# Kernel tuning notes

Measured on AMD Instinct MI355X. Metric: run time of the kernel, lower is better.

## Reference

```python
import jax, jax.numpy as jnp
import numpy as np
from jax import lax

B, N, C_IN, H, W = 256, 64, 3, 8, 8
CH = [32, 64, 128]   # cnn channels per stage
D = 128              # fc / gnn width
OUT = 5
BN_EPS = 1e-5


def setup_inputs() -> dict:
    key = jax.random.key(0)
    ks = jax.random.split(key, 24)
    x = jax.random.normal(ks[0], (B, N, C_IN, H, W), jnp.float32)
    # sparse symmetric communication graph, no self loops (GCNConv adds them)
    a = jax.random.uniform(ks[1], (B, N, N)) < 0.15
    a = jnp.logical_or(a, jnp.swapaxes(a, 1, 2)).astype(jnp.float32)
    gso = a * (1.0 - jnp.eye(N, dtype=jnp.float32))

    def lin(k, o, i):
        return (jax.random.normal(k, (o, i), jnp.float32) / np.sqrt(i)).astype(jnp.float32)

    def conv(k, o, i):
        return (jax.random.normal(k, (o, i, 3, 3), jnp.float32) / np.sqrt(i * 9)).astype(jnp.float32)

    inp = {
        'x': x, 'gso': gso,
        'w_c1': conv(ks[2], CH[0], C_IN), 'b_c1': jnp.zeros((CH[0],), jnp.float32),
        'g_bn1': jnp.ones((CH[0],), jnp.float32), 'be_bn1': jnp.zeros((CH[0],), jnp.float32),
        'w_c2': conv(ks[3], CH[1], CH[0]), 'b_c2': jnp.zeros((CH[1],), jnp.float32),
        'g_bn2': jnp.ones((CH[1],), jnp.float32), 'be_bn2': jnp.zeros((CH[1],), jnp.float32),
        'w_c3': conv(ks[4], CH[2], CH[1]), 'b_c3': jnp.zeros((CH[2],), jnp.float32),
        'g_bn3': jnp.ones((CH[2],), jnp.float32), 'be_bn3': jnp.zeros((CH[2],), jnp.float32),
        'w_fc': lin(ks[5], D, CH[2]), 'b_fc': jnp.zeros((D,), jnp.float32),
        'w_g1': lin(ks[6], D, D), 'b_g1': jnp.zeros((D,), jnp.float32),
        'w_g2': lin(ks[7], D, D), 'b_g2': jnp.zeros((D,), jnp.float32),
        'w_out': lin(ks[8], OUT, D), 'b_out': jnp.zeros((OUT,), jnp.float32),
    }
    return inp


def _cnn_block(h, w, b, g, be):
    h = lax.conv_general_dilated(h, w, (1, 1), 'SAME',
                                 dimension_numbers=('NCHW', 'OIHW', 'NCHW'))
    h = h + b[None, :, None, None]
    # eval-mode BatchNorm2d with running_mean=0, running_var=1
    h = h * (g / jnp.sqrt(1.0 + BN_EPS))[None, :, None, None] + be[None, :, None, None]
    h = jax.nn.relu(h)
    h = lax.reduce_window(h, -jnp.inf, lax.max, (1, 1, 2, 2), (1, 1, 2, 2), 'VALID')
    return h


def _forward(x, gso, w_c1, b_c1, g_bn1, be_bn1, w_c2, b_c2, g_bn2, be_bn2,
             w_c3, b_c3, g_bn3, be_bn3, w_fc, b_fc, w_g1, b_g1, w_g2, b_g2,
             w_out, b_out):
    b, n = x.shape[0], x.shape[1]
    h = x.reshape(b * n, x.shape[2], x.shape[3], x.shape[4])  # vectorize agents
    h = _cnn_block(h, w_c1, b_c1, g_bn1, be_bn1)
    h = _cnn_block(h, w_c2, b_c2, g_bn2, be_bn2)
    h = _cnn_block(h, w_c3, b_c3, g_bn3, be_bn3)          # [B*N, CH2, 1, 1]
    h = h.reshape(b * n, -1)
    h = jax.nn.relu(h @ w_fc.T + b_fc)                    # [B*N, D]
    feat = h.reshape(b, n, -1)
    # GCNConv: add self loops (weight 1), symmetric normalization
    a1 = gso + jnp.eye(n, dtype=gso.dtype)
    dinv = lax.rsqrt(a1.sum(-1))                          # deg >= 1
    ahat = dinv[:, :, None] * a1 * dinv[:, None, :]       # [B, N, N]
    hg = jax.nn.relu(jnp.einsum('bij,bjf->bif', ahat, feat @ w_g1.T) + b_g1)
    hg = jax.nn.relu(jnp.einsum('bij,bjf->bif', ahat, hg @ w_g2.T) + b_g2)
    actions = hg @ w_out.T + b_out                        # [B, N, OUT]
    return actions


def reference(x, gso, w_c1, b_c1, g_bn1, be_bn1, w_c2, b_c2, g_bn2, be_bn2,
              w_c3, b_c3, g_bn3, be_bn3, w_fc, b_fc, w_g1, b_g1, w_g2, b_g2,
              w_out, b_out):
    return _forward(x, gso, w_c1, b_c1, g_bn1, be_bn1, w_c2, b_c2, g_bn2, be_bn2,
                    w_c3, b_c3, g_bn3, be_bn3, w_fc, b_fc, w_g1, b_g1, w_g2, b_g2,
                    w_out, b_out)
```

## Files before the change

kernel.cpp:

```cpp
#include <hip/hip_runtime.h>
#include <math.h>


typedef __attribute__((ext_vector_type(8))) short bf16x8;
typedef __attribute__((ext_vector_type(4))) float f32x4;

__device__ __forceinline__ short f2bf(float f) {
  union { float f; unsigned u; } v; v.f = f;
  unsigned r = v.u + 0x7fffu + ((v.u >> 16) & 1u);
  return (short)(r >> 16);
}
__device__ __forceinline__ float bf2f(unsigned short u) {
  union { unsigned u; float f; } v; v.u = ((unsigned)u) << 16;
  return v.f;
}

__global__ __launch_bounds__(256) void pack_all(
    const float* __restrict__ w_c1, const float* __restrict__ w_c2,
    const float* __restrict__ w_c3, const float* __restrict__ w_fc,
    const float* __restrict__ w_g1, const float* __restrict__ w_g2,
    short* __restrict__ B1, short* __restrict__ B2, short* __restrict__ B3,
    short* __restrict__ Wfc, short* __restrict__ Wg1, short* __restrict__ Wg2) {
  int idx = blockIdx.x * 256 + threadIdx.x;
  if (idx < 2048) {
    int oc = idx >> 6, k = idx & 63;
    int t = k >> 2, ic = k & 3;
    float v = (t < 9 && ic < 3) ? w_c1[(oc * 3 + ic) * 9 + t] : 0.0f;
    B1[idx] = f2bf(v);
  } else if (idx < 20480) {
    int i2 = idx - 2048;
    int oc = i2 / 288, r = i2 - oc * 288;
    int t = r >> 5, ic = r & 31;
    B2[i2] = f2bf(w_c2[(oc * 32 + ic) * 9 + t]);
  } else if (idx < 94208) {
    int i3 = idx - 20480;
    int oc = i3 / 576, r = i3 - oc * 576;
    int t = r >> 6, ic = r & 63;
    B3[i3] = f2bf(w_c3[(oc * 64 + ic) * 9 + t]);
  } else if (idx < 110592) {
    int i = idx - 94208; Wfc[i] = f2bf(w_fc[i]);
  } else if (idx < 126976) {
    int i = idx - 110592; Wg1[i] = f2bf(w_g1[i]);
  } else if (idx < 143360) {
    int i = idx - 126976; Wg2[i] = f2bf(w_g2[i]);
  }
}

__global__ __launch_bounds__(256) void conv1_mfma(
    const float* __restrict__ x, const short* __restrict__ B1,
    const float* __restrict__ bias, const float* __restrict__ g,
    const float* __restrict__ be, short* __restrict__ c1) {
  __shared__ short sx[8 * 400];
  const int tid = threadIdx.x;
  const int s0 = blockIdx.x * 8;
  for (int i = tid; i < 400; i += 256)
    *(uint4*)(sx + i * 8) = (uint4){0, 0, 0, 0};
  __syncthreads();
  for (int p = tid; p < 512; p += 256) {
    const int si = p >> 6, pix = p & 63;
    const int y = pix >> 3, xx2 = pix & 7;
    const float* xb = x + (s0 + si) * 192 + pix;
    ushort4 o;
    o.x = (unsigned short)f2bf(xb[0]);
    o.y = (unsigned short)f2bf(xb[64]);
    o.z = (unsigned short)f2bf(xb[128]);
    o.w = 0;
    *(ushort4*)(sx + si * 400 + ((y + 1) * 10 + xx2 + 1) * 4) = o;
  }
  __syncthreads();
  const int lane = tid & 63, w = tid >> 6;
  const int col = lane & 15, quad = lane >> 4;
  bf16x8 Bf[2][2];
#pragma unroll
  for (int nt = 0; nt < 2; ++nt)
#pragma unroll
    for (int ks = 0; ks < 2; ++ks)
      Bf[nt][ks] = *(const bf16x8*)(B1 + (nt * 16 + col) * 64 + ks * 32 + quad * 8);
  float Abn[2], Cbn[2];
#pragma unroll
  for (int nt = 0; nt < 2; ++nt) {
    int oc = nt * 16 + col;
    float a = g[oc] * rsqrtf(1.0f + 1e-5f);
    Abn[nt] = a;
    Cbn[nt] = fmaf(bias[oc], a, be[oc]);
  }
  const int t0 = 2 * quad, t1 = t0 + 1;
  const int ky0 = t0 / 3, kx0 = t0 - 3 * (t0 / 3);
  const int ky1 = t1 / 3, kx1 = t1 - 3 * (t1 / 3);
  const int m = lane & 15;
  const int pl = m >> 2, sub = m & 3;
  const int dy = sub >> 1, dx = sub & 1;
  const uint2 z2 = {0u, 0u};
#pragma unroll
  for (int sl = 0; sl < 2; ++sl) {
    const int si = w * 2 + sl;
    const int s = s0 + si;
    const short* xb = sx + si * 400;
#pragma unroll
    for (int tile = 0; tile < 4; ++tile) {
      const int pi = tile * 4 + pl;
      const int py = pi >> 2, px = pi & 3;
      const int cy = 2 * py + dy, cx = 2 * px + dx;
      union { bf16x8 v; uint2 u[2]; } a0, a1;
      a0.u[0] = *(const uint2*)(xb + ((cy + ky0) * 10 + cx + kx0) * 4);
      a0.u[1] = *(const uint2*)(xb + ((cy + ky1) * 10 + cx + kx1) * 4);
      uint2 u8 = *(const uint2*)(xb + ((cy + 2) * 10 + cx + 2) * 4);
      a1.u[0] = (quad == 0) ? u8 : z2;
      a1.u[1] = z2;
      f32x4 acc0 = {0, 0, 0, 0}, acc1 = {0, 0, 0, 0};
      acc0 = __builtin_amdgcn_mfma_f32_16x16x32_bf16(a0.v, Bf[0][0], acc0, 0, 0, 0);
      acc0 = __builtin_amdgcn_mfma_f32_16x16x32_bf16(a1.v, Bf[0][1], acc0, 0, 0, 0);
      acc1 = __builtin_amdgcn_mfma_f32_16x16x32_bf16(a0.v, Bf[1][0], acc1, 0, 0, 0);
      acc1 = __builtin_amdgcn_mfma_f32_16x16x32_bf16(a1.v, Bf[1][1], acc1, 0, 0, 0);
      const int piq = tile * 4 + quad;
#pragma unroll
      for (int nt = 0; nt < 2; ++nt) {
        f32x4 acc = nt ? acc1 : acc0;
        float p0 = fmaf(acc[0], Abn[nt], Cbn[nt]);
        float p1 = fmaf(acc[1], Abn[nt], Cbn[nt]);
        float p2 = fmaf(acc[2], Abn[nt], Cbn[nt]);
        float p3 = fmaf(acc[3], Abn[nt], Cbn[nt]);
        float mx = fmaxf(fmaxf(fmaxf(p0, p1), fmaxf(p2, p3)), 0.0f);
        c1[s * 512 + piq * 32 + nt * 16 + col] = f2bf(mx);
      }
    }
  }
}

__global__ __launch_bounds__(256, 2) void conv2_mfma(
    const short* __restrict__ c1, const short* __restrict__ B2,
    const float* __restrict__ bias, const float* __restrict__ g,
    const float* __restrict__ be, short* __restrict__ c2) {
  __shared__ short sx[32 * 640];
  const int tid = threadIdx.x;
  const int s0 = blockIdx.x * 32;
#pragma unroll
  for (int it = 0; it < 8; ++it) {
    int c = it * 256 + tid;
    int s_l = c >> 6, k = c & 63;
    int cell = k >> 2, seg = k & 3;
    *(bf16x8*)(sx + s_l * 640 + cell * 40 + seg * 8) =
        *(const bf16x8*)(c1 + s0 * 512 + c * 8);
  }
  const int lane = tid & 63, w = tid >> 6;
  const int col = lane & 15, quad = lane >> 4;
  bf16x8 Bf[4][9];
#pragma unroll
  for (int nt = 0; nt < 4; ++nt)
#pragma unroll
    for (int t = 0; t < 9; ++t)
      Bf[nt][t] = *(const bf16x8*)(B2 + (nt * 16 + col) * 288 + t * 32 + quad * 8);
  float Abn[4], Cbn[4];
#pragma unroll
  for (int nt = 0; nt < 4; ++nt) {
    int oc = nt * 16 + col;
    float a = g[oc] * rsqrtf(1.0f + 1e-5f);
    Abn[nt] = a;
    Cbn[nt] = fmaf(bias[oc], a, be[oc]);
  }
  const int m = lane & 15;
  const int q2 = m >> 2, sub = m & 3;
  const int cy = 2 * (q2 >> 1) + (sub >> 1);
  const int cx = 2 * (q2 & 1) + (sub & 1);
  int off[9];
  bool valid[9];
#pragma unroll
  for (int t = 0; t < 9; ++t) {
    int ky = t / 3, kx = t - 3 * (t / 3);
    int yy = cy + ky - 1, xx = cx + kx - 1;
    valid[t] = ((unsigned)yy < 4u) && ((unsigned)xx < 4u);
    int yc = min(max(yy, 0), 3), xc = min(max(xx, 0), 3);
    off[t] = (yc * 4 + xc) * 40 + quad * 8;
  }
  const bf16x8 zf = {0, 0, 0, 0, 0, 0, 0, 0};
  __syncthreads();
#pragma unroll 1
  for (int si = 0; si < 8; ++si) {
    const int s_l = w * 8 + si;
    const short* ib = sx + s_l * 640;
    f32x4 acc[4];
#pragma unroll
    for (int nt = 0; nt < 4; ++nt) acc[nt] = (f32x4){0, 0, 0, 0};
#pragma unroll
    for (int t = 0; t < 9; ++t) {
      bf16x8 a = *(const bf16x8*)(ib + off[t]);
      if (!valid[t]) a = zf;
#pragma unroll
      for (int nt = 0; nt < 4; ++nt)
        acc[nt] = __builtin_amdgcn_mfma_f32_16x16x32_bf16(a, Bf[nt][t], acc[nt], 0, 0, 0);
    }
    short* ob = c2 + (s0 + s_l) * 256;
#pragma unroll
    for (int nt = 0; nt < 4; ++nt) {
      float p0 = fmaf(acc[nt][0], Abn[nt], Cbn[nt]);
      float p1 = fmaf(acc[nt][1], Abn[nt], Cbn[nt]);
      float p2 = fmaf(acc[nt][2], Abn[nt], Cbn[nt]);
      float p3 = fmaf(acc[nt][3], Abn[nt], Cbn[nt]);
      float mx = fmaxf(fmaxf(fmaxf(p0, p1), fmaxf(p2, p3)), 0.0f);
      ob[quad * 64 + nt * 16 + col] = f2bf(mx);
    }
  }
}

__global__ __launch_bounds__(256) void conv3_mfma(
    const short* __restrict__ c2, const short* __restrict__ B3,
    const float* __restrict__ bias, const float* __restrict__ g,
    const float* __restrict__ be, short* __restrict__ c3) {
  __shared__ short sB[32 * 584];
  __shared__ short sA[16 * 296];
  const int tid = threadIdx.x;
  const int s0 = blockIdx.x * 16;
#pragma unroll
  for (int it = 0; it < 2; ++it) {
    int c = it * 256 + tid;
    int s_l = c >> 5, k = c & 31;
    int cell = k >> 3, seg = k & 7;
    *(bf16x8*)(sA + s_l * 296 + cell * 72 + seg * 8) =
        *(const bf16x8*)(c2 + s0 * 256 + c * 8);
  }
  __syncthreads();
  const int lane = tid & 63, w = tid >> 6;
  const int col = lane & 15, quad = lane >> 4;
  const int m = lane & 15;
  const int cp = m & 3, sl = m >> 2;
  const int cy = cp >> 1, cx = cp & 1;
  const short* ib = sA + (w * 4 + sl) * 296;
  bf16x8 A[18];
  const bf16x8 zf = {0, 0, 0, 0, 0, 0, 0, 0};
#pragma unroll
  for (int ks = 0; ks < 18; ++ks) {
    int t = ks >> 1;
    int ky = t / 3, kx = t - 3 * (t / 3);
    int iy = cy + ky - 1, ix = cx + kx - 1;
    bool valid = ((unsigned)iy < 2u) && ((unsigned)ix < 2u);
    int iyc = min(max(iy, 0), 1), ixc = min(max(ix, 0), 1);
    bf16x8 a = *(const bf16x8*)(ib + (iyc * 2 + ixc) * 72 + (ks & 1) * 32 + quad * 8);
    A[ks] = valid ? a : zf;
  }
  f32x4 acc[8];
#pragma unroll
  for (int i = 0; i < 8; ++i) acc[i] = (f32x4){0, 0, 0, 0};
#pragma unroll
  for (int ng = 0; ng < 4; ++ng) {
    __syncthreads();
#pragma unroll
    for (int it = 0; it < 9; ++it) {
      int cidx = it * 256 + tid;
      int row = cidx / 72, seg = cidx - row * 72;
      *(bf16x8*)(sB + row * 584 + seg * 8) =
          *(const bf16x8*)(B3 + (ng * 32 + row) * 576 + seg * 8);
    }
    __syncthreads();
#pragma unroll
    for (int nt = 0; nt < 2; ++nt) {
      const int nB = (nt * 16 + col) * 584 + quad * 8;
#pragma unroll
      for (int ks = 0; ks < 18; ++ks) {
        bf16x8 b = *(const bf16x8*)(sB + nB + ks * 32);
        acc[ng * 2 + nt] =
            __builtin_amdgcn_mfma_f32_16x16x32_bf16(A[ks], b, acc[ng * 2 + nt], 0, 0, 0);
      }
    }
  }
  const int sample = s0 + w * 4 + quad;
#pragma unroll
  for (int i = 0; i < 8; ++i) {
    int oc = (i >> 1) * 32 + (i & 1) * 16 + col;
    float a = g[oc] * rsqrtf(1.0f + 1e-5f);
    float cc = fmaf(bias[oc], a, be[oc]);
    float p0 = fmaf(acc[i][0], a, cc);
    float p1 = fmaf(acc[i][1], a, cc);
    float p2 = fmaf(acc[i][2], a, cc);
    float p3 = fmaf(acc[i][3], a, cc);
    float mx = fmaxf(fmaxf(fmaxf(p0, p1), fmaxf(p2, p3)), 0.0f);
    c3[sample * 128 + oc] = f2bf(mx);
  }
}

__global__ __launch_bounds__(512) void fused_dense(
    const short* __restrict__ c3, const float* __restrict__ gso,
    const short* __restrict__ Wfc, const short* __restrict__ Wg1,
    const short* __restrict__ Wg2, const float* __restrict__ b_fc,
    const float* __restrict__ b_g1, const float* __restrict__ b_g2,
    const float* __restrict__ w_o, const float* __restrict__ b_o,
    float* __restrict__ out) {
  __shared__ short sAct[64 * 136];
  __shared__ short sT[128 * 72];
  __shared__ short sAhat[64 * 72];
  __shared__ float sDinv[64];
  __shared__ float sWo[640];
  const int tid = threadIdx.x;
  const int b = blockIdx.x;
  float* sG = (float*)sT;
  for (int i = tid; i < 4096; i += 512) sG[i] = gso[b * 4096 + i];
  for (int i = tid; i < 640; i += 512) sWo[i] = w_o[i];
  __syncthreads();
  if (tid < 64) {
    float ssum = 1.0f;
    for (int j = 0; j < 64; ++j) ssum += sG[j * 64 + tid];
    sDinv[tid] = rsqrtf(ssum);
  }
  __syncthreads();
  for (int i = tid; i < 4096; i += 512) {
    int r = i >> 6, c = i & 63;
    float v = sDinv[r] * (sG[i] + (r == c ? 1.0f : 0.0f)) * sDinv[c];
    sAhat[r * 72 + c] = f2bf(v);
  }
  for (int i = tid; i < 1024; i += 512) {
    int r = i >> 4, seg = i & 15;
    *(bf16x8*)(sAct + r * 136 + seg * 8) =
        *(const bf16x8*)(c3 + (b * 64 + r) * 128 + seg * 8);
  }
  __syncthreads();
  const int lane = tid & 63, w8 = tid >> 6;
  const int rg = w8 >> 1, nh = w8 & 1;
  const int col = lane & 15, quad = lane >> 4;
  const int arow = (rg * 16 + col) * 136;
  const int crow0 = (rg * 16 + quad * 4) * 136;
  bf16x8 A[4];
  f32x4 acc[4];

#pragma unroll
  for (int ks = 0; ks < 4; ++ks)
    A[ks] = *(const bf16x8*)(sAct + arow + ks * 32 + quad * 8);
  __syncthreads();
#pragma unroll
  for (int i = 0; i < 4; ++i) acc[i] = (f32x4){0, 0, 0, 0};
#pragma unroll
  for (int ntl = 0; ntl < 4; ++ntl) {
    const int n = (nh * 4 + ntl) * 16 + col;
#pragma unroll
    for (int ks = 0; ks < 4; ++ks) {
      bf16x8 bb = *(const bf16x8*)(Wfc + n * 128 + ks * 32 + quad * 8);
      acc[ntl] = __builtin_amdgcn_mfma_f32_16x16x32_bf16(A[ks], bb, acc[ntl], 0, 0, 0);
    }
  }
#pragma unroll
  for (int ntl = 0; ntl < 4; ++ntl) {
    const int n = (nh * 4 + ntl) * 16 + col;
    const float bv = b_fc[n];
#pragma unroll
    for (int reg = 0; reg < 4; ++reg)
      sAct[crow0 + reg * 136 + n] = f2bf(fmaxf(acc[ntl][reg] + bv, 0.0f));
  }
  __syncthreads();

#pragma unroll
  for (int ks = 0; ks < 4; ++ks)
    A[ks] = *(const bf16x8*)(sAct + arow + ks * 32 + quad * 8);
#pragma unroll
  for (int i = 0; i < 4; ++i) acc[i] = (f32x4){0, 0, 0, 0};
#pragma unroll
  for (int ntl = 0; ntl < 4; ++ntl) {
    const int n = (nh * 4 + ntl) * 16 + col;
#pragma unroll
    for (int ks = 0; ks < 4; ++ks) {
      bf16x8 bb = *(const bf16x8*)(Wg1 + n * 128 + ks * 32 + quad * 8);
      acc[ntl] = __builtin_amdgcn_mfma_f32_16x16x32_bf16(A[ks], bb, acc[ntl], 0, 0, 0);
    }
  }
#pragma unroll
  for (int ntl = 0; ntl < 4; ++ntl) {
    const int n = (nh * 4 + ntl) * 16 + col;
    ushort4 pk;
    pk.x = (unsigned short)f2bf(acc[ntl][0]);
    pk.y = (unsigned short)f2bf(acc[ntl][1]);
    pk.z = (unsigned short)f2bf(acc[ntl][2]);
    pk.w = (unsigned short)f2bf(acc[ntl][3]);
    *(ushort4*)(sT + n * 72 + rg * 16 + quad * 4) = pk;
  }
  __syncthreads();

  bf16x8 Ah[2];
#pragma unroll
  for (int ks = 0; ks < 2; ++ks)
    Ah[ks] = *(const bf16x8*)(sAhat + (rg * 16 + col) * 72 + ks * 32 + quad * 8);
#pragma unroll
  for (int i = 0; i < 4; ++i) acc[i] = (f32x4){0, 0, 0, 0};
#pragma unroll
  for (int ntl = 0; ntl < 4; ++ntl) {
    const int n = (nh * 4 + ntl) * 16 + col;
#pragma unroll
    for (int ks = 0; ks < 2; ++ks) {
      bf16x8 bb = *(const bf16x8*)(sT + n * 72 + ks * 32 + quad * 8);
      acc[ntl] = __builtin_amdgcn_mfma_f32_16x16x32_bf16(Ah[ks], bb, acc[ntl], 0, 0, 0);
    }
  }
#pragma unroll
  for (int ntl = 0; ntl < 4; ++ntl) {
    const int n = (nh * 4 + ntl) * 16 + col;
    const float bv = b_g1[n];
#pragma unroll
    for (int reg = 0; reg < 4; ++reg)
      sAct[crow0 + reg * 136 + n] = f2bf(fmaxf(acc[ntl][reg] + bv, 0.0f));
  }
  __syncthreads();

#pragma unroll
  for (int ks = 0; ks < 4; ++ks)
    A[ks] = *(const bf16x8*)(sAct + arow + ks * 32 + quad * 8);
#pragma unroll
  for (int i = 0; i < 4; ++i) acc[i] = (f32x4){0, 0, 0, 0};
#pragma unroll
  for (int ntl = 0; ntl < 4; ++ntl) {
    const int n = (nh * 4 + ntl) * 16 + col;
#pragma unroll
    for (int ks = 0; ks < 4; ++ks) {
      bf16x8 bb = *(const bf16x8*)(Wg2 + n * 128 + ks * 32 + quad * 8);
      acc[ntl] = __builtin_amdgcn_mfma_f32_16x16x32_bf16(A[ks], bb, acc[ntl], 0, 0, 0);
    }
  }
#pragma unroll
  for (int ntl = 0; ntl < 4; ++ntl) {
    const int n = (nh * 4 + ntl) * 16 + col;
    ushort4 pk;
    pk.x = (unsigned short)f2bf(acc[ntl][0]);
    pk.y = (unsigned short)f2bf(acc[ntl][1]);
    pk.z = (unsigned short)f2bf(acc[ntl][2]);
    pk.w = (unsigned short)f2bf(acc[ntl][3]);
    *(ushort4*)(sT + n * 72 + rg * 16 + quad * 4) = pk;
  }
  __syncthreads();

#pragma unroll
  for (int i = 0; i < 4; ++i) acc[i] = (f32x4){0, 0, 0, 0};
#pragma unroll
  for (int ntl = 0; ntl < 4; ++ntl) {
    const int n = (nh * 4 + ntl) * 16 + col;
#pragma unroll
    for (int ks = 0; ks < 2; ++ks) {
      bf16x8 bb = *(const bf16x8*)(sT + n * 72 + ks * 32 + quad * 8);
      acc[ntl] = __builtin_amdgcn_mfma_f32_16x16x32_bf16(Ah[ks], bb, acc[ntl], 0, 0, 0);
    }
  }
#pragma unroll
  for (int ntl = 0; ntl < 4; ++ntl) {
    const int n = (nh * 4 + ntl) * 16 + col;
    const float bv = b_g2[n];
#pragma unroll
    for (int reg = 0; reg < 4; ++reg)
      sAct[crow0 + reg * 136 + n] = f2bf(fmaxf(acc[ntl][reg] + bv, 0.0f));
  }
  __syncthreads();

  if (tid < 320) {
    const int j = tid / 5, o = tid - 5 * j;
    float a0 = 0.0f;
#pragma unroll
    for (int k8 = 0; k8 < 16; ++k8) {
      union { bf16x8 v; unsigned short u[8]; } h;
      h.v = *(const bf16x8*)(sAct + j * 136 + k8 * 8);
#pragma unroll
      for (int jj = 0; jj < 8; ++jj)
        a0 = fmaf(bf2f(h.u[jj]), sWo[o * 128 + k8 * 8 + jj], a0);
    }
    out[(b * 64 + j) * 5 + o] = a0 + b_o[o];
  }
}

extern "C" void kernel_launch(void* const* d_in, const int* in_sizes, int n_in,
                              void* d_out, int out_size, void* d_ws, size_t ws_size,
                              hipStream_t stream) {
  const float* x    = (const float*)d_in[0];
  const float* gso  = (const float*)d_in[1];
  const float* w_c1 = (const float*)d_in[2];
  const float* b_c1 = (const float*)d_in[3];
  const float* g_b1 = (const float*)d_in[4];
  const float* e_b1 = (const float*)d_in[5];
  const float* w_c2 = (const float*)d_in[6];
  const float* b_c2 = (const float*)d_in[7];
  const float* g_b2 = (const float*)d_in[8];
  const float* e_b2 = (const float*)d_in[9];
  const float* w_c3 = (const float*)d_in[10];
  const float* b_c3 = (const float*)d_in[11];
  const float* g_b3 = (const float*)d_in[12];
  const float* e_b3 = (const float*)d_in[13];
  const float* w_fc = (const float*)d_in[14];
  const float* b_fc = (const float*)d_in[15];
  const float* w_g1 = (const float*)d_in[16];
  const float* b_g1 = (const float*)d_in[17];
  const float* w_g2 = (const float*)d_in[18];
  const float* b_g2 = (const float*)d_in[19];
  const float* w_o  = (const float*)d_in[20];
  const float* b_o  = (const float*)d_in[21];
  float* out = (float*)d_out;
  char* ws = (char*)d_ws;

  short* c1  = (short*)(ws + 0);
  short* c2  = (short*)(ws + 16777216);
  short* c3  = (short*)(ws + 25165824);
  short* B1  = (short*)(ws + 29360128);
  short* B2  = (short*)(ws + 29364224);
  short* B3  = (short*)(ws + 29401088);
  short* Wfc = (short*)(ws + 29548544);
  short* Wg1 = (short*)(ws + 29581312);
  short* Wg2 = (short*)(ws + 29614080);

  pack_all<<<560, 256, 0, stream>>>(w_c1, w_c2, w_c3, w_fc, w_g1, w_g2,
                                    B1, B2, B3, Wfc, Wg1, Wg2);
  conv1_mfma<<<2048, 256, 0, stream>>>(x, B1, b_c1, g_b1, e_b1, c1);
  conv2_mfma<<<512, 256, 0, stream>>>(c1, B2, b_c2, g_b2, e_b2, c2);
  conv3_mfma<<<1024, 256, 0, stream>>>(c2, B3, b_c3, g_b3, e_b3, c3);
  fused_dense<<<256, 512, 0, stream>>>(c3, gso, Wfc, Wg1, Wg2, b_fc, b_g1,
                                       b_g2, w_o, b_o, out);
}
```

Baseline: 181.1 us.

## Fuse three conv stages into one kernel keeping intermediates in LDS

Merges conv1, conv2 and conv3 into a single kernel processing 16 samples per block, with the pooled intermediate activations held in shared memory instead of global workspace. This removes the global write and read of the c1 and c2 tensors and two kernel launches. In exchange, each block reloads the conv2 weights and stages the conv3 weights in smaller chunks with more barriers. Register and LDS pressure rise and may lower occupancy.

Result: faster. 177.1 us (-2.2%).

```diff
diff --git a/kernel.cpp b/kernel.cpp
--- a/kernel.cpp
+++ b/kernel.cpp
@@ -46,234 +46,203 @@
   }
 }
 
-__global__ __launch_bounds__(256) void conv1_mfma(
-    const float* __restrict__ x, const short* __restrict__ B1,
-    const float* __restrict__ bias, const float* __restrict__ g,
-    const float* __restrict__ be, short* __restrict__ c1) {
-  __shared__ short sx[8 * 400];
+__global__ __launch_bounds__(256, 2) void conv_all(
+    const float* __restrict__ x, const short* __restrict__ B1g,
+    const short* __restrict__ B2g, const short* __restrict__ B3g,
+    const float* __restrict__ b1, const float* __restrict__ g1,
+    const float* __restrict__ e1, const float* __restrict__ b2,
+    const float* __restrict__ g2, const float* __restrict__ e2,
+    const float* __restrict__ b3, const float* __restrict__ g3,
+    const float* __restrict__ e3, short* __restrict__ c3) {
+  __shared__ short sMix[16 * 584];
+  __shared__ short sc1[16 * 640];
+  __shared__ short sc2[16 * 296];
   const int tid = threadIdx.x;
-  const int s0 = blockIdx.x * 8;
-  for (int i = tid; i < 400; i += 256)
-    *(uint4*)(sx + i * 8) = (uint4){0, 0, 0, 0};
-  __syncthreads();
-  for (int p = tid; p < 512; p += 256) {
-    const int si = p >> 6, pix = p & 63;
-    const int y = pix >> 3, xx2 = pix & 7;
+  const int s0 = blockIdx.x * 16;
+  const int lane = tid & 63, w = tid >> 6;
+  const int col = lane & 15, quad = lane >> 4;
+  const int m = lane & 15;
+
+  for (int i = tid; i < 800; i += 256)
+    *(uint4*)(sMix + i * 8) = (uint4){0, 0, 0, 0};
+  __syncthreads();
+#pragma unroll
+  for (int it = 0; it < 4; ++it) {
+    int p = it * 256 + tid;
+    int si = p >> 6, pix = p & 63;
+    int y = pix >> 3, xx2 = pix & 7;
     const float* xb = x + (s0 + si) * 192 + pix;
     ushort4 o;
     o.x = (unsigned short)f2bf(xb[0]);
     o.y = (unsigned short)f2bf(xb[64]);
     o.z = (unsigned short)f2bf(xb[128]);
     o.w = 0;
-    *(ushort4*)(sx + si * 400 + ((y + 1) * 10 + xx2 + 1) * 4) = o;
-  }
-  __syncthreads();
-  const int lane = tid & 63, w = tid >> 6;
-  const int col = lane & 15, quad = lane >> 4;
-  bf16x8 Bf[2][2];
-#pragma unroll
-  for (int nt = 0; nt < 2; ++nt)
-#pragma unroll
-    for (int ks = 0; ks < 2; ++ks)
-      Bf[nt][ks] = *(const bf16x8*)(B1 + (nt * 16 + col) * 64 + ks * 32 + quad * 8);
-  float Abn[2], Cbn[2];
-#pragma unroll
-  for (int nt = 0; nt < 2; ++nt) {
-    int oc = nt * 16 + col;
-    float a = g[oc] * rsqrtf(1.0f + 1e-5f);
-    Abn[nt] = a;
-    Cbn[nt] = fmaf(bias[oc], a, be[oc]);
-  }
-  const int t0 = 2 * quad, t1 = t0 + 1;
-  const int ky0 = t0 / 3, kx0 = t0 - 3 * (t0 / 3);
-  const int ky1 = t1 / 3, kx1 = t1 - 3 * (t1 / 3);
-  const int m = lane & 15;
-  const int pl = m >> 2, sub = m & 3;
-  const int dy = sub >> 1, dx = sub & 1;
-  const uint2 z2 = {0u, 0u};
-#pragma unroll
-  for (int sl = 0; sl < 2; ++sl) {
-    const int si = w * 2 + sl;
-    const int s = s0 + si;
-    const short* xb = sx + si * 400;
-#pragma unroll
-    for (int tile = 0; tile < 4; ++tile) {
-      const int pi = tile * 4 + pl;
-      const int py = pi >> 2, px = pi & 3;
-      const int cy = 2 * py + dy, cx = 2 * px + dx;
-      union { bf16x8 v; uint2 u[2]; } a0, a1;
-      a0.u[0] = *(const uint2*)(xb + ((cy + ky0) * 10 + cx + kx0) * 4);
-      a0.u[1] = *(const uint2*)(xb + ((cy + ky1) * 10 + cx + kx1) * 4);
-      uint2 u8 = *(const uint2*)(xb + ((cy + 2) * 10 + cx + 2) * 4);
-      a1.u[0] = (quad == 0) ? u8 : z2;
-      a1.u[1] = z2;
-      f32x4 acc0 = {0, 0, 0, 0}, acc1 = {0, 0, 0, 0};
-      acc0 = __builtin_amdgcn_mfma_f32_16x16x32_bf16(a0.v, Bf[0][0], acc0, 0, 0, 0);
-      acc0 = __builtin_amdgcn_mfma_f32_16x16x32_bf16(a1.v, Bf[0][1], acc0, 0, 0, 0);
-      acc1 = __builtin_amdgcn_mfma_f32_16x16x32_bf16(a0.v, Bf[1][0], acc1, 0, 0, 0);
-      acc1 = __builtin_amdgcn_mfma_f32_16x16x32_bf16(a1.v, Bf[1][1], acc1, 0, 0, 0);
-      const int piq = tile * 4 + quad;
-#pragma unroll
-      for (int nt = 0; nt < 2; ++nt) {
-        f32x4 acc = nt ? acc1 : acc0;
-        float p0 = fmaf(acc[0], Abn[nt], Cbn[nt]);
-        float p1 = fmaf(acc[1], Abn[nt], Cbn[nt]);
-        float p2 = fmaf(acc[2], Abn[nt], Cbn[nt]);
-        float p3 = fmaf(acc[3], Abn[nt], Cbn[nt]);
+    *(ushort4*)(sMix + si * 400 + ((y + 1) * 10 + xx2 + 1) * 4) = o;
+  }
+  __syncthreads();
+
+  {
+    bf16x8 Bf[2][2];
+#pragma unroll
+    for (int nt = 0; nt < 2; ++nt)
+#pragma unroll
+      for (int ks = 0; ks < 2; ++ks)
+        Bf[nt][ks] = *(const bf16x8*)(B1g + (nt * 16 + col) * 64 + ks * 32 + quad * 8);
+    float Abn[2], Cbn[2];
+#pragma unroll
+    for (int nt = 0; nt < 2; ++nt) {
+      int oc = nt * 16 + col;
+      float a = g1[oc] * rsqrtf(1.0f + 1e-5f);
+      Abn[nt] = a;
+      Cbn[nt] = fmaf(b1[oc], a, e1[oc]);
+    }
+    const int t0 = 2 * quad, t1 = t0 + 1;
+    const int ky0 = t0 / 3, kx0 = t0 - 3 * (t0 / 3);
+    const int ky1 = t1 / 3, kx1 = t1 - 3 * (t1 / 3);
+    const int pl = m >> 2, sub = m & 3;
+    const int dy = sub >> 1, dx = sub & 1;
+    const uint2 z2 = {0u, 0u};
+#pragma unroll
+    for (int sl = 0; sl < 4; ++sl) {
+      const int si = w * 4 + sl;
+      const short* xb = sMix + si * 400;
+#pragma unroll
+      for (int tile = 0; tile < 4; ++tile) {
+        const int pi = tile * 4 + pl;
+        const int py = pi >> 2, px = pi & 3;
+        const int cy = 2 * py + dy, cx = 2 * px + dx;
+        union { bf16x8 v; uint2 u[2]; } a0, a1;
+        a0.u[0] = *(const uint2*)(xb + ((cy + ky0) * 10 + cx + kx0) * 4);
+        a0.u[1] = *(const uint2*)(xb + ((cy + ky1) * 10 + cx + kx1) * 4);
+        uint2 u8 = *(const uint2*)(xb + ((cy + 2) * 10 + cx + 2) * 4);
+        a1.u[0] = (quad == 0) ? u8 : z2;
+        a1.u[1] = z2;
+        f32x4 acc0 = {0, 0, 0, 0}, acc1 = {0, 0, 0, 0};
+        acc0 = __builtin_amdgcn_mfma_f32_16x16x32_bf16(a0.v, Bf[0][0], acc0, 0, 0, 0);
+        acc0 = __builtin_amdgcn_mfma_f32_16x16x32_bf16(a1.v, Bf[0][1], acc0, 0, 0, 0);
+        acc1 = __builtin_amdgcn_mfma_f32_16x16x32_bf16(a0.v, Bf[1][0], acc1, 0, 0, 0);
+        acc1 = __builtin_amdgcn_mfma_f32_16x16x32_bf16(a1.v, Bf[1][1], acc1, 0, 0, 0);
+        const int piq = tile * 4 + quad;
+#pragma unroll
+        for (int nt = 0; nt < 2; ++nt) {
+          f32x4 acc = nt ? acc1 : acc0;
+          float p0 = fmaf(acc[0], Abn[nt], Cbn[nt]);
+          float p1 = fmaf(acc[1], Abn[nt], Cbn[nt]);
+          float p2 = fmaf(acc[2], Abn[nt], Cbn[nt]);
+          float p3 = fmaf(acc[3], Abn[nt], Cbn[nt]);
+          float mx = fmaxf(fmaxf(fmaxf(p0, p1), fmaxf(p2, p3)), 0.0f);
+          sc1[si * 640 + piq * 40 + nt * 16 + col] = f2bf(mx);
+        }
+      }
+    }
+  }
+  __syncthreads();
+
+  {
+    bf16x8 Bf[4][9];
+#pragma unroll
+    for (int nt = 0; nt < 4; ++nt)
+#pragma unroll
+      for (int t = 0; t < 9; ++t)
+        Bf[nt][t] = *(const bf16x8*)(B2g + (nt * 16 + col) * 288 + t * 32 + quad * 8);
+    float Abn[4], Cbn[4];
+#pragma unroll
+    for (int nt = 0; nt < 4; ++nt) {
+      int oc = nt * 16 + col;
+      float a = g2[oc] * rsqrtf(1.0f + 1e-5f);
+      Abn[nt] = a;
+      Cbn[nt] = fmaf(b2[oc], a, e2[oc]);
+    }
+    const int q2 = m >> 2, sub = m & 3;
+    const int cy = 2 * (q2 >> 1) + (sub >> 1);
+    const int cx = 2 * (q2 & 1) + (sub & 1);
+    int off[9];
+    bool valid[9];
+#pragma unroll
+    for (int t = 0; t < 9; ++t) {
+      int ky = t / 3, kx = t - 3 * (t / 3);
+      int yy = cy + ky - 1, xx = cx + kx - 1;
+      valid[t] = ((unsigned)yy < 4u) && ((unsigned)xx < 4u);
+      int yc = min(max(yy, 0), 3), xc = min(max(xx, 0), 3);
+      off[t] = (yc * 4 + xc) * 40 + quad * 8;
+    }
+    const bf16x8 zf = {0, 0, 0, 0, 0, 0, 0, 0};
+#pragma unroll
+    for (int sl = 0; sl < 4; ++sl) {
+      const int si = w * 4 + sl;
+      const short* ib = sc1 + si * 640;
+      f32x4 acc[4];
+#pragma unroll
+      for (int nt = 0; nt < 4; ++nt) acc[nt] = (f32x4){0, 0, 0, 0};
+#pragma unroll
+      for (int t = 0; t < 9; ++t) {
+        bf16x8 a = *(const bf16x8*)(ib + off[t]);
+        if (!valid[t]) a = zf;
+#pragma unroll
+        for (int nt = 0; nt < 4; ++nt)
+          acc[nt] = __builtin_amdgcn_mfma_f32_16x16x32_bf16(a, Bf[nt][t], acc[nt], 0, 0, 0);
+      }
+#pragma unroll
+      for (int nt = 0; nt < 4; ++nt) {
+        float p0 = fmaf(acc[nt][0], Abn[nt], Cbn[nt]);
+        float p1 = fmaf(acc[nt][1], Abn[nt], Cbn[nt]);
+        float p2 = fmaf(acc[nt][2], Abn[nt], Cbn[nt]);
+        float p3 = fmaf(acc[nt][3], Abn[nt], Cbn[nt]);
         float mx = fmaxf(fmaxf(fmaxf(p0, p1), fmaxf(p2, p3)), 0.0f);
-        c1[s * 512 + piq * 32 + nt * 16 + col] = f2bf(mx);
+        sc2[si * 296 + quad * 72 + nt * 16 + col] = f2bf(mx);
       }
     }
   }
-}
-
-__global__ __launch_bounds__(256, 2) void conv2_mfma(
-    const short* __restrict__ c1, const short* __restrict__ B2,
-    const float* __restrict__ bias, const float* __restrict__ g,
-    const float* __restrict__ be, short* __restrict__ c2) {
-  __shared__ short sx[32 * 640];
-  const int tid = threadIdx.x;
-  const int s0 = blockIdx.x * 32;
-#pragma unroll
-  for (int it = 0; it < 8; ++it) {
-    int c = it * 256 + tid;
-    int s_l = c >> 6, k = c & 63;
-    int cell = k >> 2, seg = k & 3;
-    *(bf16x8*)(sx + s_l * 640 + cell * 40 + seg * 8) =
-        *(const bf16x8*)(c1 + s0 * 512 + c * 8);
-  }
-  const int lane = tid & 63, w = tid >> 6;
-  const int col = lane & 15, quad = lane >> 4;
-  bf16x8 Bf[4][9];
-#pragma unroll
-  for (int nt = 0; nt < 4; ++nt)
-#pragma unroll
-    for (int t = 0; t < 9; ++t)
-      Bf[nt][t] = *(const bf16x8*)(B2 + (nt * 16 + col) * 288 + t * 32 + quad * 8);
-  float Abn[4], Cbn[4];
-#pragma unroll
-  for (int nt = 0; nt < 4; ++nt) {
-    int oc = nt * 16 + col;
-    float a = g[oc] * rsqrtf(1.0f + 1e-5f);
-    Abn[nt] = a;
-    Cbn[nt] = fmaf(bias[oc], a, be[oc]);
-  }
-  const int m = lane & 15;
-  const int q2 = m >> 2, sub = m & 3;
-  const int cy = 2 * (q2 >> 1) + (sub >> 1);
-  const int cx = 2 * (q2 & 1) + (sub & 1);
-  int off[9];
-  bool valid[9];
-#pragma unroll
-  for (int t = 0; t < 9; ++t) {
-    int ky = t / 3, kx = t - 3 * (t / 3);
-    int yy = cy + ky - 1, xx = cx + kx - 1;
-    valid[t] = ((unsigned)yy < 4u) && ((unsigned)xx < 4u);
-    int yc = min(max(yy, 0), 3), xc = min(max(xx, 0), 3);
-    off[t] = (yc * 4 + xc) * 40 + quad * 8;
-  }
-  const bf16x8 zf = {0, 0, 0, 0, 0, 0, 0, 0};
-  __syncthreads();
+  __syncthreads();
+
+  {
+    const int cp = m & 3, sl3 = m >> 2;
+    const int cy = cp >> 1, cx = cp & 1;
+    const short* ib = sc2 + (w * 4 + sl3) * 296;
+    bf16x8 A[18];
+    const bf16x8 zf = {0, 0, 0, 0, 0, 0, 0, 0};
+#pragma unroll
+    for (int ks = 0; ks < 18; ++ks) {
+      int t = ks >> 1;
+      int ky = t / 3, kx = t - 3 * (t / 3);
+      int iy = cy + ky - 1, ix = cx + kx - 1;
+      bool valid = ((unsigned)iy < 2u) && ((unsigned)ix < 2u);
+      int iyc = min(max(iy, 0), 1), ixc = min(max(ix, 0), 1);
+      bf16x8 a = *(const bf16x8*)(ib + (iyc * 2 + ixc) * 72 + (ks & 1) * 32 + quad * 8);
+      A[ks] = valid ? a : zf;
+    }
+    f32x4 acc[8];
+#pragma unroll
+    for (int i = 0; i < 8; ++i) acc[i] = (f32x4){0, 0, 0, 0};
 #pragma unroll 1
-  for (int si = 0; si < 8; ++si) {
-    const int s_l = w * 8 + si;
-    const short* ib = sx + s_l * 640;
-    f32x4 acc[4];
-#pragma unroll
-    for (int nt = 0; nt < 4; ++nt) acc[nt] = (f32x4){0, 0, 0, 0};
-#pragma unroll
-    for (int t = 0; t < 9; ++t) {
-      bf16x8 a = *(const bf16x8*)(ib + off[t]);
-      if (!valid[t]) a = zf;
-#pragma unroll
-      for (int nt = 0; nt < 4; ++nt)
-        acc[nt] = __builtin_amdgcn_mfma_f32_16x16x32_bf16(a, Bf[nt][t], acc[nt], 0, 0, 0);
-    }
-    short* ob = c2 + (s0 + s_l) * 256;
-#pragma unroll
-    for (int nt = 0; nt < 4; ++nt) {
-      float p0 = fmaf(acc[nt][0], Abn[nt], Cbn[nt]);
-      float p1 = fmaf(acc[nt][1], Abn[nt], Cbn[nt]);
-      float p2 = fmaf(acc[nt][2], Abn[nt], Cbn[nt]);
-      float p3 = fmaf(acc[nt][3], Abn[nt], Cbn[nt]);
+    for (int ng = 0; ng < 8; ++ng) {
+      __syncthreads();
+      for (int c = tid; c < 1152; c += 256) {
+        int row = c / 72, seg = c - row * 72;
+        *(bf16x8*)(sMix + row * 584 + seg * 8) =
+            *(const bf16x8*)(B3g + (ng * 16 + row) * 576 + seg * 8);
+      }
+      __syncthreads();
+      const int nB = col * 584 + quad * 8;
+#pragma unroll
+      for (int ks = 0; ks < 18; ++ks) {
+        bf16x8 b = *(const bf16x8*)(sMix + nB + ks * 32);
+        acc[ng] = __builtin_amdgcn_mfma_f32_16x16x32_bf16(A[ks], b, acc[ng], 0, 0, 0);
+      }
+    }
+    const int sample = s0 + w * 4 + quad;
+#pragma unroll
+    for (int ng = 0; ng < 8; ++ng) {
+      int oc = ng * 16 + col;
+      float a = g3[oc] * rsqrtf(1.0f + 1e-5f);
+      float cc = fmaf(b3[oc], a, e3[oc]);
+      float p0 = fmaf(acc[ng][0], a, cc);
+      float p1 = fmaf(acc[ng][1], a, cc);
+      float p2 = fmaf(acc[ng][2], a, cc);
+      float p3 = fmaf(acc[ng][3], a, cc);
       float mx = fmaxf(fmaxf(fmaxf(p0, p1), fmaxf(p2, p3)), 0.0f);
-      ob[quad * 64 + nt * 16 + col] = f2bf(mx);
-    }
-  }
-}
-
-__global__ __launch_bounds__(256) void conv3_mfma(
-    const short* __restrict__ c2, const short* __restrict__ B3,
-    const float* __restrict__ bias, const float* __restrict__ g,
-    const float* __restrict__ be, short* __restrict__ c3) {
-  __shared__ short sB[32 * 584];
-  __shared__ short sA[16 * 296];
-  const int tid = threadIdx.x;
-  const int s0 = blockIdx.x * 16;
-#pragma unroll
-  for (int it = 0; it < 2; ++it) {
-    int c = it * 256 + tid;
-    int s_l = c >> 5, k = c & 31;
-    int cell = k >> 3, seg = k & 7;
-    *(bf16x8*)(sA + s_l * 296 + cell * 72 + seg * 8) =
-        *(const bf16x8*)(c2 + s0 * 256 + c * 8);
-  }
-  __syncthreads();
-  const int lane = tid & 63, w = tid >> 6;
-  const int col = lane & 15, quad = lane >> 4;
-  const int m = lane & 15;
-  const int cp = m & 3, sl = m >> 2;
-  const int cy = cp >> 1, cx = cp & 1;
-  const short* ib = sA + (w * 4 + sl) * 296;
-  bf16x8 A[18];
-  const bf16x8 zf = {0, 0, 0, 0, 0, 0, 0, 0};
-#pragma unroll
-  for (int ks = 0; ks < 18; ++ks) {
-    int t = ks >> 1;
-    int ky = t / 3, kx = t - 3 * (t / 3);
-    int iy = cy + ky - 1, ix = cx + kx - 1;
-    bool valid = ((unsigned)iy < 2u) && ((unsigned)ix < 2u);
-    int iyc = min(max(iy, 0), 1), ixc = min(max(ix, 0), 1);
-    bf16x8 a = *(const bf16x8*)(ib + (iyc * 2 + ixc) * 72 + (ks & 1) * 32 + quad * 8);
-    A[ks] = valid ? a : zf;
-  }
-  f32x4 acc[8];
-#pragma unroll
-  for (int i = 0; i < 8; ++i) acc[i] = (f32x4){0, 0, 0, 0};
-#pragma unroll
-  for (int ng = 0; ng < 4; ++ng) {
-    __syncthreads();
-#pragma unroll
-    for (int it = 0; it < 9; ++it) {
-      int cidx = it * 256 + tid;
-      int row = cidx / 72, seg = cidx - row * 72;
-      *(bf16x8*)(sB + row * 584 + seg * 8) =
-          *(const bf16x8*)(B3 + (ng * 32 + row) * 576 + seg * 8);
-    }
-    __syncthreads();
-#pragma unroll
-    for (int nt = 0; nt < 2; ++nt) {
-      const int nB = (nt * 16 + col) * 584 + quad * 8;
-#pragma unroll
-      for (int ks = 0; ks < 18; ++ks) {
-        bf16x8 b = *(const bf16x8*)(sB + nB + ks * 32);
-        acc[ng * 2 + nt] =
-            __builtin_amdgcn_mfma_f32_16x16x32_bf16(A[ks], b, acc[ng * 2 + nt], 0, 0, 0);
-      }
-    }
-  }
-  const int sample = s0 + w * 4 + quad;
-#pragma unroll
-  for (int i = 0; i < 8; ++i) {
-    int oc = (i >> 1) * 32 + (i & 1) * 16 + col;
-    float a = g[oc] * rsqrtf(1.0f + 1e-5f);
-    float cc = fmaf(bias[oc], a, be[oc]);
-    float p0 = fmaf(acc[i][0], a, cc);
-    float p1 = fmaf(acc[i][1], a, cc);
-    float p2 = fmaf(acc[i][2], a, cc);
-    float p3 = fmaf(acc[i][3], a, cc);
-    float mx = fmaxf(fmaxf(fmaxf(p0, p1), fmaxf(p2, p3)), 0.0f);
-    c3[sample * 128 + oc] = f2bf(mx);
+      c3[sample * 128 + oc] = f2bf(mx);
+    }
   }
 }
 
@@ -486,21 +455,18 @@
   float* out = (float*)d_out;
   char* ws = (char*)d_ws;
 
-  short* c1  = (short*)(ws + 0);
-  short* c2  = (short*)(ws + 16777216);
-  short* c3  = (short*)(ws + 25165824);
-  short* B1  = (short*)(ws + 29360128);
-  short* B2  = (short*)(ws + 29364224);
-  short* B3  = (short*)(ws + 29401088);
-  short* Wfc = (short*)(ws + 29548544);
-  short* Wg1 = (short*)(ws + 29581312);
-  short* Wg2 = (short*)(ws + 29614080);
+  short* c3  = (short*)(ws + 0);
+  short* B1  = (short*)(ws + 4194304);
+  short* B2  = (short*)(ws + 4198400);
+  short* B3  = (short*)(ws + 4235264);
+  short* Wfc = (short*)(ws + 4382720);
+  short* Wg1 = (short*)(ws + 4415488);
+  short* Wg2 = (short*)(ws + 4448256);
 
   pack_all<<<560, 256, 0, stream>>>(w_c1, w_c2, w_c3, w_fc, w_g1, w_g2,
                                     B1, B2, B3, Wfc, Wg1, Wg2);
-  conv1_mfma<<<2048, 256, 0, stream>>>(x, B1, b_c1, g_b1, e_b1, c1);
-  conv2_mfma<<<512, 256, 0, stream>>>(c1, B2, b_c2, g_b2, e_b2, c2);
-  conv3_mfma<<<1024, 256, 0, stream>>>(c2, B3, b_c3, g_b3, e_b3, c3);
+  conv_all<<<1024, 256, 0, stream>>>(x, B1, B2, B3, b_c1, g_b1, e_b1,
+                                     b_c2, g_b2, e_b2, b_c3, g_b3, e_b3, c3);
   fused_dense<<<256, 512, 0, stream>>>(c3, gso, Wfc, Wg1, Wg2, b_fc, b_g1,
                                        b_g2, w_o, b_o, out);
 }
```
